# Performance work log

Hardware: AMD Instinct MI355X
Metric: run time of the kernel (lower is better)

Reference implementation:

```python
import jax, jax.numpy as jnp
import numpy as np

D_MODEL = 1024
N_HEADS = 16
N_GROUPS = 4
D_K = D_MODEL // N_HEADS
HEADS_PER_GROUP = N_HEADS // N_GROUPS


def rope(x):
    # x: [b, s, d]; rotate using half-split concat (NOT interleaved), matching source
    s, d = x.shape[1], x.shape[2]
    theta = 1.0 / (10000.0 ** (jnp.arange(d // 2, dtype=jnp.float32) / (d // 2)))
    ang = jnp.arange(s, dtype=jnp.float32)[:, None] * theta[None, :]  # [s, d/2]
    cos, sin = jnp.cos(ang), jnp.sin(ang)
    xe, xo = x[..., 0::2], x[..., 1::2]
    return jnp.concatenate([xe * cos - xo * sin, xe * sin + xo * cos], axis=-1)


def setup_inputs() -> dict:
    key = jax.random.key(0)
    k1, k2, k3, k4, k5 = jax.random.split(key, 5)
    b, s = 1, 2048
    scale = 0.02
    X = jax.random.normal(k1, (b, s, D_MODEL), dtype=jnp.float32)
    W_q = jax.random.normal(k2, (D_MODEL, D_MODEL), dtype=jnp.float32) * scale
    W_k = jax.random.normal(k3, (N_GROUPS * D_K, D_MODEL), dtype=jnp.float32) * scale
    W_v = jax.random.normal(k4, (N_GROUPS * D_K, D_MODEL), dtype=jnp.float32) * scale
    W_o = jax.random.normal(k5, (D_MODEL, D_MODEL), dtype=jnp.float32) * scale
    return {"X": X, "W_q": W_q, "W_k": W_k, "W_v": W_v, "W_o": W_o}


def reference(X, W_q, W_k, W_v, W_o):
    b, s, _ = X.shape
    Xr = rope(X)
    Q = (Xr @ W_q.T).reshape(b, s, N_HEADS, D_K).transpose(0, 2, 1, 3)
    K = (Xr @ W_k.T).reshape(b, s, N_GROUPS, D_K).transpose(0, 2, 1, 3)
    V = (Xr @ W_v.T).reshape(b, s, N_GROUPS, D_K).transpose(0, 2, 1, 3)
    Q = Q.reshape(b, N_GROUPS, HEADS_PER_GROUP, s, D_K)
    scores = jnp.einsum('bghsd,bgtd->bghst', Q, K) / jnp.sqrt(jnp.float32(D_K))
    mask = jnp.triu(jnp.ones((s, s), dtype=scores.dtype), k=1) * (-1e9)
    attn = jax.nn.softmax(scores + mask, axis=-1)
    out = jnp.einsum('bghst,bgtd->bghsd', attn, V)  # [b,g,h,s,dk]
    out = out.reshape(b, N_HEADS, s, D_K).transpose(0, 2, 1, 3).reshape(b, s, D_MODEL)
    return out @ W_o.T
```

## Files before the change

### kernel.cpp

```cpp
#include <hip/hip_runtime.h>
#include <hip/hip_bf16.h>

#define S_LEN   2048
#define D_MODEL 1024
#define N_HEADS 16
#define N_GROUPS 4
#define D_K     64
#define KV_DIM  (N_GROUPS * D_K)

typedef __hip_bfloat16 bf16;
typedef unsigned short u16;
typedef __attribute__((ext_vector_type(8))) short bfrag;
typedef __attribute__((ext_vector_type(4))) float ffrag;
typedef __attribute__((ext_vector_type(4))) unsigned int u32x4;

__device__ __forceinline__ float b2f(u16 u) {
    return __uint_as_float(((unsigned)u) << 16);
}
__device__ __forceinline__ u16 f2bu(float f) {
    bf16 h = __float2bfloat16(f);
    return __builtin_bit_cast(u16, h);
}
__device__ __forceinline__ unsigned cvt_pk_bf16(float lo, float hi) {
    unsigned r;
    asm("v_cvt_pk_bf16_f32 %0, %1, %2" : "=v"(r) : "v"(lo), "v"(hi));
    return r;
}
__device__ __forceinline__ float max3f(float a, float b, float c) {
    float d;
    asm("v_max3_f32 %0, %1, %2, %3" : "=v"(d) : "v"(a), "v"(b), "v"(c));
    return d;
}
__device__ __forceinline__ float ex2(float x) {
#if __has_builtin(__builtin_amdgcn_exp2f)
    return __builtin_amdgcn_exp2f(x);
#else
    return __expf(x * 0.69314718f);
#endif
}

typedef __attribute__((address_space(3))) u16 lds_u16;
typedef __attribute__((address_space(1))) const u16 glb_u16;
__device__ __forceinline__ void gld_lds16(const u16* g, u16* l) {
    __builtin_amdgcn_global_load_lds((glb_u16*)g, (lds_u16*)l, 16, 0, 0);
}

__device__ __forceinline__ int posCS3(int i, int c) {
    if (i >= 4 * c + 3)
        return (c == 0) ? i - 3 : (c == 1) ? i + 6 : (c == 2) ? i + 11 : 27;
    int dd = i - 4 * c + 1;
    return 28 + (3 - dd) * 4 + c;
}

__device__ __forceinline__ int probe_f32(const u16* p) {
    int lane = threadIdx.x & 63;
    int e0 = (p[lane] >> 7) & 0xFF;
    int e1 = (p[lane + 64] >> 7) & 0xFF;
    int c = ((e0 < 100 || e0 > 140) ? 1 : 0) + ((e1 < 100 || e1 > 140) ? 1 : 0);
    unsigned long long b1 = __ballot(c >= 1);
    unsigned long long b2 = __ballot(c >= 2);
    return ((__popcll(b1) + __popcll(b2)) > 16) ? 1 : 0;
}

__global__ void probe5_kernel(const u16* __restrict__ p0, const u16* __restrict__ p1,
                              const u16* __restrict__ p2, const u16* __restrict__ p3,
                              const u16* __restrict__ p4, int* __restrict__ mode) {
    if (blockIdx.x != 0) return;
    const u16* ps[5] = {p0, p1, p2, p3, p4};
    int lane = threadIdx.x & 63;
    for (int t = 0; t < 5; t++) {
        int e0 = (ps[t][lane] >> 7) & 0xFF;
        int e1 = (ps[t][lane + 64] >> 7) & 0xFF;
        int c = ((e0 < 100 || e0 > 140) ? 1 : 0) + ((e1 < 100 || e1 > 140) ? 1 : 0);
        unsigned long long b1 = __ballot(c >= 1);
        unsigned long long b2 = __ballot(c >= 2);
        if (lane == 0) mode[t] = ((__popcll(b1) + __popcll(b2)) > 16) ? 1 : 0;
    }
}

__global__ __launch_bounds__(512)
void prep_kernel(const void* __restrict__ Xin, u16* __restrict__ Xr,
                 const void* __restrict__ Wq, const void* __restrict__ Wk,
                 const void* __restrict__ Wv, const void* __restrict__ Wo,
                 u16* __restrict__ WB, u16* __restrict__ WoB) {
    int b = blockIdx.x;
    if (b < S_LEN) {
        int md = probe_f32((const u16*)Xin);
        int i = b;
        int j = threadIdx.x;
        float freq = ex2(-(float)j * 0.025952563241307518f);
        float ang  = (float)i * freq;
        float sv, cv;
        sincosf(ang, &sv, &cv);
        int base = i * D_MODEL;
        float xe, xo;
        if (md) {
            float2 xv = *(const float2*)&((const float*)Xin)[base + 2 * j];
            xe = xv.x; xo = xv.y;
        } else {
            ushort2 xv = *(const ushort2*)&((const u16*)Xin)[base + 2 * j];
            xe = b2f(xv.x); xo = b2f(xv.y);
        }
        Xr[base + j]       = f2bu(xe * cv - xo * sv);
        Xr[base + 512 + j] = f2bu(xe * sv + xo * cv);
    } else {
        int bid = b - S_LEN;
        const void* src; u16* dst; int goff;
        if (bid < 256)      { src = Wq; dst = WB;               goff = bid; }
        else if (bid < 320) { src = Wk; dst = WB + 1024 * 1024; goff = bid - 256; }
        else if (bid < 384) { src = Wv; dst = WB + 1280 * 1024; goff = bid - 320; }
        else                { src = Wo; dst = WoB;              goff = bid - 384; }
        int md = probe_f32((const u16*)src);
        size_t g = (size_t)goff * 512 + threadIdx.x;
        if (md) {
            const float* f = (const float*)src + g * 8;
            float4 v0 = *(const float4*)f;
            float4 v1 = *(const float4*)(f + 4);
            u16 t[8] = {f2bu(v0.x), f2bu(v0.y), f2bu(v0.z), f2bu(v0.w),
                        f2bu(v1.x), f2bu(v1.y), f2bu(v1.z), f2bu(v1.w)};
            *(uint4*)(dst + g * 8) = *(const uint4*)t;
        } else {
            *(uint4*)(dst + g * 8) = *(const uint4*)((const u16*)src + g * 8);
        }
    }
}

__global__ __launch_bounds__(512)
void rope_kernel(const void* __restrict__ Xin, u16* __restrict__ Xr) {
    int md = probe_f32((const u16*)Xin);
    int i = blockIdx.x;
    int j = threadIdx.x;
    float freq = ex2(-(float)j * 0.025952563241307518f);
    float ang  = (float)i * freq;
    float sv, cv;
    sincosf(ang, &sv, &cv);
    int base = i * D_MODEL;
    float xe, xo;
    if (md) {
        float2 xv = *(const float2*)&((const float*)Xin)[base + 2 * j];
        xe = xv.x; xo = xv.y;
    } else {
        ushort2 xv = *(const ushort2*)&((const u16*)Xin)[base + 2 * j];
        xe = b2f(xv.x); xo = b2f(xv.y);
    }
    Xr[base + j]       = f2bu(xe * cv - xo * sv);
    Xr[base + 512 + j] = f2bu(xe * sv + xo * cv);
}

template<int MODE>
__global__ __launch_bounds__(256)
void gemm_fast(const u16* __restrict__ A, const u16* __restrict__ WBm,
               u16* __restrict__ Qm, u16* __restrict__ Km, u16* __restrict__ Vm,
               float* __restrict__ Cf) {
    __shared__ u16 As[2][8192];
    __shared__ u16 Bs[2][4096];
    const int tid = threadIdx.x;
    const int w = tid >> 6, lane = tid & 63, quad = lane >> 4, lcol = lane & 15;

    const int flat = blockIdx.y * gridDim.x + blockIdx.x;
    const int cpx  = (gridDim.x * gridDim.y) >> 3;
    const int ns   = (flat & 7) * cpx + (flat >> 3);
    const int m0 = (ns / gridDim.x) * 128;
    const int n0 = (ns % gridDim.x) * 64;

    const int arl   = lane >> 3;
    const int colsw = ((lane & 7) ^ arl) * 8;

    const u16* ap[4]; const u16* bp[2];
    #pragma unroll
    for (int c = 0; c < 4; c++)
        ap[c] = A + (size_t)(m0 + (c * 4 + w) * 8 + arl) * 1024 + colsw;
    #pragma unroll
    for (int c = 0; c < 2; c++)
        bp[c] = WBm + (size_t)(n0 + (c * 4 + w) * 8 + arl) * 1024 + colsw;

    const int abase = (w * 32 + lcol) * 64;
    const int koff0 = (quad * 8) ^ ((lcol & 7) * 8);
    const int koff1 = koff0 ^ 32;

    ffrag acc[2][4];
    #pragma unroll
    for (int rf = 0; rf < 2; rf++)
        #pragma unroll
        for (int ct = 0; ct < 4; ct++) acc[rf][ct] = (ffrag)0.0f;

    #pragma unroll
    for (int c = 0; c < 4; c++) gld_lds16(ap[c], &As[0][(c * 4 + w) * 512]);
    #pragma unroll
    for (int c = 0; c < 2; c++) gld_lds16(bp[c], &Bs[0][(c * 4 + w) * 512]);
    __syncthreads();

    int cur = 0;
    for (int k0 = 0; k0 < D_MODEL; k0 += 64) {
        if (k0 + 64 < D_MODEL) {
            const int nb = cur ^ 1;
            #pragma unroll
            for (int c = 0; c < 4; c++)
                gld_lds16(ap[c] + k0 + 64, &As[nb][(c * 4 + w) * 512]);
            #pragma unroll
            for (int c = 0; c < 2; c++)
                gld_lds16(bp[c] + k0 + 64, &Bs[nb][(c * 4 + w) * 512]);
        }

        const u16* Ab = &As[cur][0];
        const u16* Bb = &Bs[cur][0];
        const bfrag a00 = *(const bfrag*)&Ab[abase + koff0];
        const bfrag a10 = *(const bfrag*)&Ab[abase + 1024 + koff0];
        const bfrag a01 = *(const bfrag*)&Ab[abase + koff1];
        const bfrag a11 = *(const bfrag*)&Ab[abase + 1024 + koff1];
        #pragma unroll
        for (int ct = 0; ct < 4; ct++) {
            const int bb = (ct * 16 + lcol) * 64;
            const bfrag b0 = *(const bfrag*)&Bb[bb + koff0];
            acc[0][ct] = __builtin_amdgcn_mfma_f32_16x16x32_bf16(a00, b0, acc[0][ct], 0, 0, 0);
            acc[1][ct] = __builtin_amdgcn_mfma_f32_16x16x32_bf16(a10, b0, acc[1][ct], 0, 0, 0);
            const bfrag b1 = *(const bfrag*)&Bb[bb + koff1];
            acc[0][ct] = __builtin_amdgcn_mfma_f32_16x16x32_bf16(a01, b1, acc[0][ct], 0, 0, 0);
            acc[1][ct] = __builtin_amdgcn_mfma_f32_16x16x32_bf16(a11, b1, acc[1][ct], 0, 0, 0);
        }
        __syncthreads();
        cur ^= 1;
    }

    if (MODE == 0) {
        if (n0 < 1280) {
            u16* Cp; int ldc, nc;
            if (n0 < 1024) { Cp = Qm; ldc = 1024; nc = n0; }
            else           { Cp = Km; ldc = 256;  nc = n0 - 1024; }
            #pragma unroll
            for (int rf = 0; rf < 2; rf++)
                #pragma unroll
                for (int ct = 0; ct < 4; ct++)
                    #pragma unroll
                    for (int r = 0; r < 4; r++) {
                        int row = m0 + w * 32 + rf * 16 + quad * 4 + r;
                        Cp[(size_t)row * ldc + nc + ct * 16 + lcol] = f2bu(acc[rf][ct][r]);
                    }
        } else {
            const int nc = n0 - 1280;
            #pragma unroll
            for (int rf = 0; rf < 2; rf++)
                #pragma unroll
                for (int ct = 0; ct < 4; ct++)
                    #pragma unroll
                    for (int r = 0; r < 4; r++) {
                        int row = m0 + w * 32 + rf * 16 + quad * 4 + r;
                        int col = nc + ct * 16 + lcol;
                        Vm[(size_t)col * S_LEN + row] = f2bu(acc[rf][ct][r]);
                    }
        }
    } else {
        #pragma unroll
        for (int rf = 0; rf < 2; rf++)
            #pragma unroll
            for (int ct = 0; ct < 4; ct++)
                #pragma unroll
                for (int r = 0; r < 4; r++) {
                    int row = m0 + w * 32 + rf * 16 + quad * 4 + r;
                    Cf[(size_t)row * D_MODEL + n0 + ct * 16 + lcol] = acc[rf][ct][r];
                }
    }
}

__device__ __forceinline__ void stageB(u16* dst, const void* Bv, size_t off, int md) {
    if (md) {
        const float* Bf = (const float*)Bv;
        float4 b0 = *(const float4*)&Bf[off];
        float4 b1 = *(const float4*)&Bf[off + 4];
        u16 t[8] = {f2bu(b0.x), f2bu(b0.y), f2bu(b0.z), f2bu(b0.w),
                    f2bu(b1.x), f2bu(b1.y), f2bu(b1.z), f2bu(b1.w)};
        *(uint4*)dst = *(const uint4*)t;
    } else {
        *(uint4*)dst = *(const uint4*)&((const u16*)Bv)[off];
    }
}

__global__ __launch_bounds__(256)
void qkv_mfma(const u16* __restrict__ Xr, const void* __restrict__ Wq,
              const void* __restrict__ Wk, const void* __restrict__ Wv,
              u16* __restrict__ Qm, u16* __restrict__ Km, u16* __restrict__ Vm,
              const int* __restrict__ mode) {
    __shared__ u16 As[128][36];
    __shared__ u16 Bs[64][36];
    const int tid = threadIdx.x;
    const int w = tid >> 6, lane = tid & 63, quad = lane >> 4, lcol = lane & 15;
    const int m0 = blockIdx.y * 128;
    const int n0 = blockIdx.x * 64;

    const void* Bv; int nb, md;
    if (n0 < 1024)       { Bv = Wq; nb = n0;        md = mode[1]; }
    else if (n0 < 1280)  { Bv = Wk; nb = n0 - 1024; md = mode[2]; }
    else                 { Bv = Wv; nb = n0 - 1280; md = mode[3]; }

    ffrag acc[2][4];
    #pragma unroll
    for (int rf = 0; rf < 2; rf++)
        #pragma unroll
        for (int ct = 0; ct < 4; ct++) acc[rf][ct] = (ffrag)0.0f;

    const int arow = tid >> 2, akc = tid & 3;
    for (int k0 = 0; k0 < D_MODEL; k0 += 32) {
        *(uint4*)&As[arow][akc * 8] =
            *(const uint4*)&Xr[(size_t)(m0 + arow) * D_MODEL + k0 + akc * 8];
        *(uint4*)&As[arow + 64][akc * 8] =
            *(const uint4*)&Xr[(size_t)(m0 + arow + 64) * D_MODEL + k0 + akc * 8];
        stageB(&Bs[arow][akc * 8], Bv, (size_t)(nb + arow) * D_MODEL + k0 + akc * 8, md);
        __syncthreads();
        const bfrag a0 = *(const bfrag*)&As[w * 32 + lcol][quad * 8];
        const bfrag a1 = *(const bfrag*)&As[w * 32 + 16 + lcol][quad * 8];
        #pragma unroll
        for (int ct = 0; ct < 4; ct++) {
            const bfrag b = *(const bfrag*)&Bs[ct * 16 + lcol][quad * 8];
            acc[0][ct] = __builtin_amdgcn_mfma_f32_16x16x32_bf16(a0, b, acc[0][ct], 0, 0, 0);
            acc[1][ct] = __builtin_amdgcn_mfma_f32_16x16x32_bf16(a1, b, acc[1][ct], 0, 0, 0);
        }
        __syncthreads();
    }

    if (n0 < 1280) {
        u16* Cp; int ldc, nc;
        if (n0 < 1024) { Cp = Qm; ldc = 1024; nc = n0; }
        else           { Cp = Km; ldc = 256;  nc = n0 - 1024; }
        #pragma unroll
        for (int rf = 0; rf < 2; rf++)
            #pragma unroll
            for (int ct = 0; ct < 4; ct++)
                #pragma unroll
                for (int r = 0; r < 4; r++) {
                    int row = m0 + w * 32 + rf * 16 + quad * 4 + r;
                    Cp[(size_t)row * ldc + nc + ct * 16 + lcol] = f2bu(acc[rf][ct][r]);
                }
    } else {
        const int nc = n0 - 1280;
        #pragma unroll
        for (int rf = 0; rf < 2; rf++)
            #pragma unroll
            for (int ct = 0; ct < 4; ct++)
                #pragma unroll
                for (int r = 0; r < 4; r++) {
                    int row = m0 + w * 32 + rf * 16 + quad * 4 + r;
                    int col = nc + ct * 16 + lcol;
                    Vm[(size_t)col * S_LEN + row] = f2bu(acc[rf][ct][r]);
                }
    }
}

__global__ __launch_bounds__(256)
void oproj_mfma(const u16* __restrict__ A, const void* __restrict__ B,
                float* __restrict__ C, const int* __restrict__ mode) {
    __shared__ u16 As[128][36];
    __shared__ u16 Bs[64][36];
    const int tid = threadIdx.x;
    const int w = tid >> 6, lane = tid & 63, quad = lane >> 4, lcol = lane & 15;
    const int m0 = blockIdx.y * 128;
    const int n0 = blockIdx.x * 64;
    const int md = mode[4];

    ffrag acc[2][4];
    #pragma unroll
    for (int rf = 0; rf < 2; rf++)
        #pragma unroll
        for (int ct = 0; ct < 4; ct++) acc[rf][ct] = (ffrag)0.0f;

    const int arow = tid >> 2, akc = tid & 3;
    for (int k0 = 0; k0 < D_MODEL; k0 += 32) {
        *(uint4*)&As[arow][akc * 8] =
            *(const uint4*)&A[(size_t)(m0 + arow) * D_MODEL + k0 + akc * 8];
        *(uint4*)&As[arow + 64][akc * 8] =
            *(const uint4*)&A[(size_t)(m0 + arow + 64) * D_MODEL + k0 + akc * 8];
        stageB(&Bs[arow][akc * 8], B, (size_t)(n0 + arow) * D_MODEL + k0 + akc * 8, md);
        __syncthreads();
        const bfrag a0 = *(const bfrag*)&As[w * 32 + lcol][quad * 8];
        const bfrag a1 = *(const bfrag*)&As[w * 32 + 16 + lcol][quad * 8];
        #pragma unroll
        for (int ct = 0; ct < 4; ct++) {
            const bfrag b = *(const bfrag*)&Bs[ct * 16 + lcol][quad * 8];
            acc[0][ct] = __builtin_amdgcn_mfma_f32_16x16x32_bf16(a0, b, acc[0][ct], 0, 0, 0);
            acc[1][ct] = __builtin_amdgcn_mfma_f32_16x16x32_bf16(a1, b, acc[1][ct], 0, 0, 0);
        }
        __syncthreads();
    }

    #pragma unroll
    for (int rf = 0; rf < 2; rf++)
        #pragma unroll
        for (int ct = 0; ct < 4; ct++)
            #pragma unroll
            for (int r = 0; r < 4; r++) {
                int row = m0 + w * 32 + rf * 16 + quad * 4 + r;
                C[(size_t)row * D_MODEL + n0 + ct * 16 + lcol] = acc[rf][ct][r];
            }
}

template<int CS, int SF>
__global__ __launch_bounds__(256, 4)
void attn_part(const u16* __restrict__ Q, const u16* __restrict__ K,
               const u16* __restrict__ Vt, float* __restrict__ OpF,
               u16* __restrict__ OpH, float2* __restrict__ ml2) {
    const int bid = blockIdx.x;
    const int cidx = bid >> 4;
    const int h = bid & 15;
    const int g = h >> 2;

    int i, c;
    if (CS == 3) {
        if (cidx < 13)       { c = 0; i = cidx + 3; }
        else if (cidx < 22)  { c = 1; i = cidx - 6; }
        else if (cidx < 27)  { c = 2; i = cidx - 11; }
        else if (cidx == 27) { c = 3; i = 15; }
        else { int t = cidx - 28; int dd = 3 - (t >> 2); c = t & 3; i = 4 * c + dd - 1; }
    } else {
        if (cidx < 8) { i = cidx; c = 0; }
        else          { i = 8 + ((cidx - 8) >> 1); c = (cidx - 8) & 1; }
    }
    const int i0 = i * 128;
    const int tile0 = c << CS;
    const int tlast = min(2 * i + 1, ((c + 1) << CS) - 1);
    const int nt = tlast - tile0 + 1;

    const int tid  = threadIdx.x;
    const int w    = tid >> 6;
    const int lane = tid & 63;
    const int quad = lane >> 4;
    const int lcol = lane & 15;

    __shared__ u16 Ks[2][64][72];
    __shared__ u16 Vts[2][64][72];

    const int qiA = i0 + w * 16 + lcol;
    const int qiB = qiA + 64;
    const bfrag qbA0 = *(const bfrag*)&Q[(size_t)qiA * D_MODEL + h * 64 + quad * 8];
    const bfrag qbA1 = *(const bfrag*)&Q[(size_t)qiA * D_MODEL + h * 64 + 32 + quad * 8];
    const bfrag qbB0 = *(const bfrag*)&Q[(size_t)qiB * D_MODEL + h * 64 + quad * 8];
    const bfrag qbB1 = *(const bfrag*)&Q[(size_t)qiB * D_MODEL + h * 64 + 32 + quad * 8];

    ffrag oaccA[4], oaccB[4];
    #pragma unroll
    for (int ct = 0; ct < 4; ct++) { oaccA[ct] = (ffrag)0.0f; oaccB[ct] = (ffrag)0.0f; }
    float m_runA = 0.0f, l_runA = 0.0f;
    float m_runB = 0.0f, l_runB = 0.0f;

    const int key0 = tid & 63, dc0 = tid >> 6;
    const int vd0 = tid >> 3, vch = tid & 7;
    const int vpos0 = 32 * (vch >> 2) + 16 * (vch & 1) + 4 * ((vch >> 1) & 1);
    const u16* vbase0 = &Vt[(size_t)(g * 64 + vd0) * S_LEN];
    const u16* vbase1 = &Vt[(size_t)(g * 64 + vd0 + 32) * S_LEN];

    int jp = tile0 * 64;
    uint4 kpre0 = *(const uint4*)&K[(size_t)(jp + key0) * KV_DIM + g * 64 + dc0 * 8];
    uint4 kpre1 = *(const uint4*)&K[(size_t)(jp + key0) * KV_DIM + g * 64 + (dc0 + 4) * 8];
    uint4 vpre0 = *(const uint4*)&vbase0[jp + vch * 8];
    uint4 vpre1 = *(const uint4*)&vbase1[jp + vch * 8];

    {
        *(uint4*)&Ks[0][key0][dc0 * 8]       = kpre0;
        *(uint4*)&Ks[0][key0][(dc0 + 4) * 8] = kpre1;
        *(uint2*)&Vts[0][vd0][vpos0]          = make_uint2(vpre0.x, vpre0.y);
        *(uint2*)&Vts[0][vd0][vpos0 + 8]      = make_uint2(vpre0.z, vpre0.w);
        *(uint2*)&Vts[0][vd0 + 32][vpos0]     = make_uint2(vpre1.x, vpre1.y);
        *(uint2*)&Vts[0][vd0 + 32][vpos0 + 8] = make_uint2(vpre1.z, vpre1.w);
    }

    const float CF = 0.18033688f;
    int cur = 0;

    for (int tt = 0; tt < nt; tt++) {
        const int tj = tile0 + tt;
        const int j0 = tj * 64;

        if (tt + 1 < nt) {
            const int j0n = (tj + 1) * 64;
            kpre0 = *(const uint4*)&K[(size_t)(j0n + key0) * KV_DIM + g * 64 + dc0 * 8];
            kpre1 = *(const uint4*)&K[(size_t)(j0n + key0) * KV_DIM + g * 64 + (dc0 + 4) * 8];
            vpre0 = *(const uint4*)&vbase0[j0n + vch * 8];
            vpre1 = *(const uint4*)&vbase1[j0n + vch * 8];
        }
        __syncthreads();

        ffrag saccA[4], saccB[4];
        #pragma unroll
        for (int ct = 0; ct < 4; ct++) { saccA[ct] = (ffrag)0.0f; saccB[ct] = (ffrag)0.0f; }
        __builtin_amdgcn_s_setprio(1);
        #pragma unroll
        for (int ct = 0; ct < 4; ct++) {
            const bfrag kb0 = *(const bfrag*)&Ks[cur][ct * 16 + lcol][quad * 8];
            saccA[ct] = __builtin_amdgcn_mfma_f32_16x16x32_bf16(kb0, qbA0, saccA[ct], 0, 0, 0);
            saccB[ct] = __builtin_amdgcn_mfma_f32_16x16x32_bf16(kb0, qbB0, saccB[ct], 0, 0, 0);
            const bfrag kb1 = *(const bfrag*)&Ks[cur][ct * 16 + lcol][32 + quad * 8];
            saccA[ct] = __builtin_amdgcn_mfma_f32_16x16x32_bf16(kb1, qbA1, saccA[ct], 0, 0, 0);
            saccB[ct] = __builtin_amdgcn_mfma_f32_16x16x32_bf16(kb1, qbB1, saccB[ct], 0, 0, 0);
        }
        __builtin_amdgcn_s_setprio(0);

        float svA[4][4];
        if (tj >= 2 * i) {
            #pragma unroll
            for (int ct = 0; ct < 4; ct++)
                #pragma unroll
                for (int r = 0; r < 4; r++) {
                    int kj = j0 + ct * 16 + quad * 4 + r;
                    svA[ct][r] = (kj <= qiA) ? saccA[ct][r] : -1e30f;
                }
        } else {
            #pragma unroll
            for (int ct = 0; ct < 4; ct++)
                #pragma unroll
                for (int r = 0; r < 4; r++) svA[ct][r] = saccA[ct][r];
        }
        float tA0 = max3f(svA[0][0], svA[0][1], svA[0][2]);
        float tA1 = max3f(svA[0][3], svA[1][0], svA[1][1]);
        float tA2 = max3f(svA[1][2], svA[1][3], svA[2][0]);
        float tA3 = max3f(svA[2][1], svA[2][2], svA[2][3]);
        float tA4 = max3f(svA[3][0], svA[3][1], svA[3][2]);
        float mxA = fmaxf(max3f(tA0, tA1, tA2), max3f(tA3, tA4, svA[3][3]));
        mxA = fmaxf(mxA, __shfl_xor(mxA, 16, 64));
        mxA = fmaxf(mxA, __shfl_xor(mxA, 32, 64));

        const float mcA = m_runA * CF;
        float rsA = 0.0f;
        #pragma unroll
        for (int ct = 0; ct < 4; ct++)
            #pragma unroll
            for (int r = 0; r < 4; r++) {
                float p = ex2(svA[ct][r] * CF - mcA);
                svA[ct][r] = p;
                rsA += p;
            }
        rsA += __shfl_xor(rsA, 16, 64);
        rsA += __shfl_xor(rsA, 32, 64);
        l_runA += rsA;

        u32x4 pwA0, pwA1;
        pwA0[0] = cvt_pk_bf16(svA[0][0], svA[0][1]);
        pwA0[1] = cvt_pk_bf16(svA[0][2], svA[0][3]);
        pwA0[2] = cvt_pk_bf16(svA[1][0], svA[1][1]);
        pwA0[3] = cvt_pk_bf16(svA[1][2], svA[1][3]);
        pwA1[0] = cvt_pk_bf16(svA[2][0], svA[2][1]);
        pwA1[1] = cvt_pk_bf16(svA[2][2], svA[2][3]);
        pwA1[2] = cvt_pk_bf16(svA[3][0], svA[3][1]);
        pwA1[3] = cvt_pk_bf16(svA[3][2], svA[3][3]);
        const bfrag paA0 = __builtin_bit_cast(bfrag, pwA0);
        const bfrag paA1 = __builtin_bit_cast(bfrag, pwA1);

        float svB[4][4];
        if (tj == 2 * i + 1) {
            #pragma unroll
            for (int ct = 0; ct < 4; ct++)
                #pragma unroll
                for (int r = 0; r < 4; r++) {
                    int kj = j0 + ct * 16 + quad * 4 + r;
                    svB[ct][r] = (kj <= qiB) ? saccB[ct][r] : -1e30f;
                }
        } else {
            #pragma unroll
            for (int ct = 0; ct < 4; ct++)
                #pragma unroll
                for (int r = 0; r < 4; r++) svB[ct][r] = saccB[ct][r];
        }
        float tB0 = max3f(svB[0][0], svB[0][1], svB[0][2]);
        float tB1 = max3f(svB[0][3], svB[1][0], svB[1][1]);
        float tB2 = max3f(svB[1][2], svB[1][3], svB[2][0]);
        float tB3 = max3f(svB[2][1], svB[2][2], svB[2][3]);
        float tB4 = max3f(svB[3][0], svB[3][1], svB[3][2]);
        float mxB = fmaxf(max3f(tB0, tB1, tB2), max3f(tB3, tB4, svB[3][3]));
        mxB = fmaxf(mxB, __shfl_xor(mxB, 16, 64));
        mxB = fmaxf(mxB, __shfl_xor(mxB, 32, 64));

        const float mcB = m_runB * CF;
        float rsB = 0.0f;
        #pragma unroll
        for (int ct = 0; ct < 4; ct++)
            #pragma unroll
            for (int r = 0; r < 4; r++) {
                float p = ex2(svB[ct][r] * CF - mcB);
                svB[ct][r] = p;
                rsB += p;
            }
        rsB += __shfl_xor(rsB, 16, 64);
        rsB += __shfl_xor(rsB, 32, 64);
        l_runB += rsB;

        u32x4 pwB0, pwB1;
        pwB0[0] = cvt_pk_bf16(svB[0][0], svB[0][1]);
        pwB0[1] = cvt_pk_bf16(svB[0][2], svB[0][3]);
        pwB0[2] = cvt_pk_bf16(svB[1][0], svB[1][1]);
        pwB0[3] = cvt_pk_bf16(svB[1][2], svB[1][3]);
        pwB1[0] = cvt_pk_bf16(svB[2][0], svB[2][1]);
        pwB1[1] = cvt_pk_bf16(svB[2][2], svB[2][3]);
        pwB1[2] = cvt_pk_bf16(svB[3][0], svB[3][1]);
        pwB1[3] = cvt_pk_bf16(svB[3][2], svB[3][3]);
        const bfrag paB0 = __builtin_bit_cast(bfrag, pwB0);
        const bfrag paB1 = __builtin_bit_cast(bfrag, pwB1);

        __builtin_amdgcn_s_setprio(1);
        #pragma unroll
        for (int ct = 0; ct < 4; ct++) {
            const bfrag vb0 = *(const bfrag*)&Vts[cur][ct * 16 + lcol][quad * 8];
            oaccA[ct] = __builtin_amdgcn_mfma_f32_16x16x32_bf16(paA0, vb0, oaccA[ct], 0, 0, 0);
            oaccB[ct] = __builtin_amdgcn_mfma_f32_16x16x32_bf16(paB0, vb0, oaccB[ct], 0, 0, 0);
            const bfrag vb1 = *(const bfrag*)&Vts[cur][ct * 16 + lcol][32 + quad * 8];
            oaccA[ct] = __builtin_amdgcn_mfma_f32_16x16x32_bf16(paA1, vb1, oaccA[ct], 0, 0, 0);
            oaccB[ct] = __builtin_amdgcn_mfma_f32_16x16x32_bf16(paB1, vb1, oaccB[ct], 0, 0, 0);
        }
        __builtin_amdgcn_s_setprio(0);

        if (!__all(mxA <= m_runA + 44.0f)) {
            float mnew = fmaxf(m_runA, mxA);
            float al = ex2((m_runA - mnew) * CF);
            l_runA *= al;
            #pragma unroll
            for (int r = 0; r < 4; r++) {
                float ar = __shfl(al, quad * 4 + r, 64);
                #pragma unroll
                for (int ct = 0; ct < 4; ct++) oaccA[ct][r] *= ar;
            }
            m_runA = mnew;
        }
        if (!__all(mxB <= m_runB + 44.0f)) {
            float mnew = fmaxf(m_runB, mxB);
            float al = ex2((m_runB - mnew) * CF);
            l_runB *= al;
            #pragma unroll
            for (int r = 0; r < 4; r++) {
                float ar = __shfl(al, quad * 4 + r, 64);
                #pragma unroll
                for (int ct = 0; ct < 4; ct++) oaccB[ct][r] *= ar;
            }
            m_runB = mnew;
        }

        if (tt + 1 < nt) {
            const int nb = cur ^ 1;
            *(uint4*)&Ks[nb][key0][dc0 * 8]       = kpre0;
            *(uint4*)&Ks[nb][key0][(dc0 + 4) * 8] = kpre1;
            *(uint2*)&Vts[nb][vd0][vpos0]          = make_uint2(vpre0.x, vpre0.y);
            *(uint2*)&Vts[nb][vd0][vpos0 + 8]      = make_uint2(vpre0.z, vpre0.w);
            *(uint2*)&Vts[nb][vd0 + 32][vpos0]     = make_uint2(vpre1.x, vpre1.y);
            *(uint2*)&Vts[nb][vd0 + 32][vpos0 + 8] = make_uint2(vpre1.z, vpre1.w);
        }
        cur ^= 1;
    }

    #pragma unroll
    for (int ct = 0; ct < 4; ct++)
        #pragma unroll
        for (int r = 0; r < 4; r++) {
            int rowA = w * 16 + quad * 4 + r;
            size_t offA = (size_t)bid * 8192 + rowA * 64 + ct * 16 + lcol;
            size_t offB = offA + 4096;
            if (SF) { OpF[offA] = oaccA[ct][r]; OpF[offB] = oaccB[ct][r]; }
            else    { OpH[offA] = f2bu(oaccA[ct][r]); OpH[offB] = f2bu(oaccB[ct][r]); }
        }
    if (quad == 0) {
        ml2[(size_t)bid * 128 + w * 16 + lcol]      = make_float2(m_runA * 0.125f, l_runA);
        ml2[(size_t)bid * 128 + 64 + w * 16 + lcol] = make_float2(m_runB * 0.125f, l_runB);
    }
}

template<int CS, int SF>
__global__ __launch_bounds__(256)
void attn_combine(const float* __restrict__ OpF, const u16* __restrict__ OpH,
                  const float2* __restrict__ ml2, u16* __restrict__ Om) {
    const int row = blockIdx.x;
    const int i = row >> 7;
    const int r = row & 127;
    const int t = threadIdx.x;
    const int h = t >> 4;
    const int d = (t & 15) * 4;
    const int nc = (CS == 3) ? ((2 * i + 1) >> 3) + 1 : ((2 * i + 1) >> 4) + 1;

    float M = -1e30f;
    for (int c = 0; c < nc; c++) {
        int pos = (CS == 3) ? posCS3(i, c) : ((i < 8) ? i : 8 + 2 * (i - 8) + c);
        float2 m = ml2[(size_t)(pos * 16 + h) * 128 + r];
        M = fmaxf(M, m.x);
    }
    float L = 0.0f;
    float acc[4] = {0.0f, 0.0f, 0.0f, 0.0f};
    for (int c = 0; c < nc; c++) {
        int pos = (CS == 3) ? posCS3(i, c) : ((i < 8) ? i : 8 + 2 * (i - 8) + c);
        float2 m = ml2[(size_t)(pos * 16 + h) * 128 + r];
        float wgt = __expf(m.x - M);
        L += m.y * wgt;
        size_t off = (size_t)(pos * 16 + h) * 8192 + r * 64 + d;
        if (SF) {
            float4 v = *(const float4*)&OpF[off];
            acc[0] += v.x * wgt; acc[1] += v.y * wgt;
            acc[2] += v.z * wgt; acc[3] += v.w * wgt;
        } else {
            ushort4 v = *(const ushort4*)&OpH[off];
            acc[0] += b2f(v.x) * wgt; acc[1] += b2f(v.y) * wgt;
            acc[2] += b2f(v.z) * wgt; acc[3] += b2f(v.w) * wgt;
        }
    }
    float inv = 1.0f / L;
    #pragma unroll
    for (int k = 0; k < 4; k++)
        Om[(size_t)row * D_MODEL + h * 64 + d + k] = f2bu(acc[k] * inv);
}

extern "C" void kernel_launch(void* const* d_in, const int* in_sizes, int n_in,
                              void* d_out, int out_size, void* d_ws, size_t ws_size,
                              hipStream_t stream) {
    const void* X  = d_in[0];
    const void* Wq = d_in[1];
    const void* Wk = d_in[2];
    const void* Wv = d_in[3];
    const void* Wo = d_in[4];
    float* out = (float*)d_out;

    u16* XrB = (u16*)d_out;

    int* mode = (int*)d_ws;
    u16* Qm = (u16*)((char*)d_ws + 64);
    u16* Km = Qm + (size_t)S_LEN * D_MODEL;
    u16* Vm = Km + (size_t)S_LEN * KV_DIM;
    u16* Om = Vm + (size_t)S_LEN * KV_DIM;

    const size_t needA    = 10485824ULL + 20971520ULL + 655360ULL;
    const size_t needFull = needA + 3145728ULL + 2097152ULL;

    if (ws_size >= needFull) {
        float*  OpF = (float*)((char*)d_ws + 10485824);
        float2* ml2 = (float2*)((char*)d_ws + 10485824 + 20971520);
        u16*    WB  = (u16*)((char*)d_ws + needA);
        u16*    WoB = WB + (size_t)1536 * 1024;

        prep_kernel<<<S_LEN + 640, 512, 0, stream>>>(X, XrB, Wq, Wk, Wv, Wo, WB, WoB);
        gemm_fast<0><<<dim3(24, 16), 256, 0, stream>>>(XrB, WB, Qm, Km, Vm, nullptr);
        attn_part<3, 1><<<40 * 16, 256, 0, stream>>>(Qm, Km, Vm, OpF, nullptr, ml2);
        attn_combine<3, 1><<<S_LEN, 256, 0, stream>>>(OpF, nullptr, ml2, Om);
        gemm_fast<1><<<dim3(16, 16), 256, 0, stream>>>(Om, WoB, nullptr, nullptr, nullptr, out);
    } else {
        rope_kernel<<<S_LEN, 512, 0, stream>>>(X, XrB);
        probe5_kernel<<<1, 64, 0, stream>>>(
            (const u16*)X, (const u16*)Wq, (const u16*)Wk, (const u16*)Wv,
            (const u16*)Wo, mode);
        qkv_mfma<<<dim3((D_MODEL + 2 * KV_DIM) / 64, S_LEN / 128), 256, 0, stream>>>(
            XrB, Wq, Wk, Wv, Qm, Km, Vm, mode);
        if (ws_size >= needA) {
            float*  OpF = (float*)((char*)d_ws + 10485824);
            float2* ml2 = (float2*)((char*)d_ws + 10485824 + 20971520);
            attn_part<3, 1><<<40 * 16, 256, 0, stream>>>(Qm, Km, Vm, OpF, nullptr, ml2);
            attn_combine<3, 1><<<S_LEN, 256, 0, stream>>>(OpF, nullptr, ml2, Om);
        } else {
            u16*    OpH = (u16*)d_out;
            float2* ml2 = (float2*)((char*)d_out + (size_t)768 * 4096 * 2);
            attn_part<4, 0><<<24 * 16, 256, 0, stream>>>(Qm, Km, Vm, nullptr, OpH, ml2);
            attn_combine<4, 0><<<S_LEN, 256, 0, stream>>>(nullptr, OpH, ml2, Om);
        }
        oproj_mfma<<<dim3(D_MODEL / 64, S_LEN / 128), 256, 0, stream>>>(Om, Wo, out, mode);
    }
}
```

Baseline: 136.4 us.

## Skip fully-masked A-row tiles and widen lazy softmax rescale threshold

Adds a per-tile hasA flag so that key tiles lying entirely beyond the A query block's causal range skip that block's QK and PV MFMAs and its softmax work. The lazy max-rescale now runs before exponentiation, uses a per-lane max with a wave vote before the cross-lane shuffle reduction, and its threshold rises from 44 to 550. Occupancy hint drops from 4 to 3 waves per SIMD to give the compiler more registers. The larger threshold lets ex2 arguments reach large values (around 99 in log2 units), which risks overflow in fp32 accumulators for inputs with big score spreads, and the split code paths add branching.

```diff
diff --git a/kernel.cpp b/kernel.cpp
--- a/kernel.cpp
+++ b/kernel.cpp
@@ -393,7 +393,7 @@
 }
 
 template<int CS, int SF>
-__global__ __launch_bounds__(256, 4)
+__global__ __launch_bounds__(256, 3)
 void attn_part(const u16* __restrict__ Q, const u16* __restrict__ K,
                const u16* __restrict__ Vt, float* __restrict__ OpF,
                u16* __restrict__ OpH, float2* __restrict__ ml2) {
@@ -462,11 +462,13 @@
     }
 
     const float CF = 0.18033688f;
+    const float GRD = 550.0f;
     int cur = 0;
 
     for (int tt = 0; tt < nt; tt++) {
         const int tj = tile0 + tt;
         const int j0 = tj * 64;
+        const bool hasA = (tj <= 2 * i);
 
         if (tt + 1 < nt) {
             const int j0n = (tj + 1) * 64;
@@ -481,66 +483,90 @@
         #pragma unroll
         for (int ct = 0; ct < 4; ct++) { saccA[ct] = (ffrag)0.0f; saccB[ct] = (ffrag)0.0f; }
         __builtin_amdgcn_s_setprio(1);
-        #pragma unroll
-        for (int ct = 0; ct < 4; ct++) {
-            const bfrag kb0 = *(const bfrag*)&Ks[cur][ct * 16 + lcol][quad * 8];
-            saccA[ct] = __builtin_amdgcn_mfma_f32_16x16x32_bf16(kb0, qbA0, saccA[ct], 0, 0, 0);
-            saccB[ct] = __builtin_amdgcn_mfma_f32_16x16x32_bf16(kb0, qbB0, saccB[ct], 0, 0, 0);
-            const bfrag kb1 = *(const bfrag*)&Ks[cur][ct * 16 + lcol][32 + quad * 8];
-            saccA[ct] = __builtin_amdgcn_mfma_f32_16x16x32_bf16(kb1, qbA1, saccA[ct], 0, 0, 0);
-            saccB[ct] = __builtin_amdgcn_mfma_f32_16x16x32_bf16(kb1, qbB1, saccB[ct], 0, 0, 0);
+        if (hasA) {
+            #pragma unroll
+            for (int ct = 0; ct < 4; ct++) {
+                const bfrag kb0 = *(const bfrag*)&Ks[cur][ct * 16 + lcol][quad * 8];
+                saccA[ct] = __builtin_amdgcn_mfma_f32_16x16x32_bf16(kb0, qbA0, saccA[ct], 0, 0, 0);
+                saccB[ct] = __builtin_amdgcn_mfma_f32_16x16x32_bf16(kb0, qbB0, saccB[ct], 0, 0, 0);
+                const bfrag kb1 = *(const bfrag*)&Ks[cur][ct * 16 + lcol][32 + quad * 8];
+                saccA[ct] = __builtin_amdgcn_mfma_f32_16x16x32_bf16(kb1, qbA1, saccA[ct], 0, 0, 0);
+                saccB[ct] = __builtin_amdgcn_mfma_f32_16x16x32_bf16(kb1, qbB1, saccB[ct], 0, 0, 0);
+            }
+        } else {
+            #pragma unroll
+            for (int ct = 0; ct < 4; ct++) {
+                const bfrag kb0 = *(const bfrag*)&Ks[cur][ct * 16 + lcol][quad * 8];
+                saccB[ct] = __builtin_amdgcn_mfma_f32_16x16x32_bf16(kb0, qbB0, saccB[ct], 0, 0, 0);
+                const bfrag kb1 = *(const bfrag*)&Ks[cur][ct * 16 + lcol][32 + quad * 8];
+                saccB[ct] = __builtin_amdgcn_mfma_f32_16x16x32_bf16(kb1, qbB1, saccB[ct], 0, 0, 0);
+            }
         }
         __builtin_amdgcn_s_setprio(0);
 
-        float svA[4][4];
-        if (tj >= 2 * i) {
+        bfrag paA0, paA1;
+        if (hasA) {
+            float svA[4][4];
+            if (tj == 2 * i) {
+                #pragma unroll
+                for (int ct = 0; ct < 4; ct++)
+                    #pragma unroll
+                    for (int r = 0; r < 4; r++) {
+                        int kj = j0 + ct * 16 + quad * 4 + r;
+                        svA[ct][r] = (kj <= qiA) ? saccA[ct][r] : -1e30f;
+                    }
+            } else {
+                #pragma unroll
+                for (int ct = 0; ct < 4; ct++)
+                    #pragma unroll
+                    for (int r = 0; r < 4; r++) svA[ct][r] = saccA[ct][r];
+            }
+            float tA0 = max3f(svA[0][0], svA[0][1], svA[0][2]);
+            float tA1 = max3f(svA[0][3], svA[1][0], svA[1][1]);
+            float tA2 = max3f(svA[1][2], svA[1][3], svA[2][0]);
+            float tA3 = max3f(svA[2][1], svA[2][2], svA[2][3]);
+            float tA4 = max3f(svA[3][0], svA[3][1], svA[3][2]);
+            float lA = fmaxf(max3f(tA0, tA1, tA2), max3f(tA3, tA4, svA[3][3]));
+            if (!__all(lA <= m_runA + GRD)) {
+                float mx = fmaxf(lA, __shfl_xor(lA, 16, 64));
+                mx = fmaxf(mx, __shfl_xor(mx, 32, 64));
+                float mnew = fmaxf(m_runA, mx);
+                float al = ex2((m_runA - mnew) * CF);
+                l_runA *= al;
+                #pragma unroll
+                for (int r = 0; r < 4; r++) {
+                    float ar = __shfl(al, quad * 4 + r, 64);
+                    #pragma unroll
+                    for (int ct = 0; ct < 4; ct++) oaccA[ct][r] *= ar;
+                }
+                m_runA = mnew;
+            }
+            const float mcA = m_runA * CF;
+            float rsA = 0.0f;
             #pragma unroll
             for (int ct = 0; ct < 4; ct++)
                 #pragma unroll
                 for (int r = 0; r < 4; r++) {
-                    int kj = j0 + ct * 16 + quad * 4 + r;
-                    svA[ct][r] = (kj <= qiA) ? saccA[ct][r] : -1e30f;
+                    float p = ex2(svA[ct][r] * CF - mcA);
+                    svA[ct][r] = p;
+                    rsA += p;
                 }
-        } else {
-            #pragma unroll
-            for (int ct = 0; ct < 4; ct++)
-                #pragma unroll
-                for (int r = 0; r < 4; r++) svA[ct][r] = saccA[ct][r];
-        }
-        float tA0 = max3f(svA[0][0], svA[0][1], svA[0][2]);
-        float tA1 = max3f(svA[0][3], svA[1][0], svA[1][1]);
-        float tA2 = max3f(svA[1][2], svA[1][3], svA[2][0]);
-        float tA3 = max3f(svA[2][1], svA[2][2], svA[2][3]);
-        float tA4 = max3f(svA[3][0], svA[3][1], svA[3][2]);
-        float mxA = fmaxf(max3f(tA0, tA1, tA2), max3f(tA3, tA4, svA[3][3]));
-        mxA = fmaxf(mxA, __shfl_xor(mxA, 16, 64));
-        mxA = fmaxf(mxA, __shfl_xor(mxA, 32, 64));
-
-        const float mcA = m_runA * CF;
-        float rsA = 0.0f;
-        #pragma unroll
-        for (int ct = 0; ct < 4; ct++)
-            #pragma unroll
-            for (int r = 0; r < 4; r++) {
-                float p = ex2(svA[ct][r] * CF - mcA);
-                svA[ct][r] = p;
-                rsA += p;
-            }
-        rsA += __shfl_xor(rsA, 16, 64);
-        rsA += __shfl_xor(rsA, 32, 64);
-        l_runA += rsA;
-
-        u32x4 pwA0, pwA1;
-        pwA0[0] = cvt_pk_bf16(svA[0][0], svA[0][1]);
-        pwA0[1] = cvt_pk_bf16(svA[0][2], svA[0][3]);
-        pwA0[2] = cvt_pk_bf16(svA[1][0], svA[1][1]);
-        pwA0[3] = cvt_pk_bf16(svA[1][2], svA[1][3]);
-        pwA1[0] = cvt_pk_bf16(svA[2][0], svA[2][1]);
-        pwA1[1] = cvt_pk_bf16(svA[2][2], svA[2][3]);
-        pwA1[2] = cvt_pk_bf16(svA[3][0], svA[3][1]);
-        pwA1[3] = cvt_pk_bf16(svA[3][2], svA[3][3]);
-        const bfrag paA0 = __builtin_bit_cast(bfrag, pwA0);
-        const bfrag paA1 = __builtin_bit_cast(bfrag, pwA1);
+            rsA += __shfl_xor(rsA, 16, 64);
+            rsA += __shfl_xor(rsA, 32, 64);
+            l_runA += rsA;
+
+            u32x4 pwA0, pwA1;
+            pwA0[0] = cvt_pk_bf16(svA[0][0], svA[0][1]);
+            pwA0[1] = cvt_pk_bf16(svA[0][2], svA[0][3]);
+            pwA0[2] = cvt_pk_bf16(svA[1][0], svA[1][1]);
+            pwA0[3] = cvt_pk_bf16(svA[1][2], svA[1][3]);
+            pwA1[0] = cvt_pk_bf16(svA[2][0], svA[2][1]);
+            pwA1[1] = cvt_pk_bf16(svA[2][2], svA[2][3]);
+            pwA1[2] = cvt_pk_bf16(svA[3][0], svA[3][1]);
+            pwA1[3] = cvt_pk_bf16(svA[3][2], svA[3][3]);
+            paA0 = __builtin_bit_cast(bfrag, pwA0);
+            paA1 = __builtin_bit_cast(bfrag, pwA1);
+        }
 
         float svB[4][4];
         if (tj == 2 * i + 1) {
@@ -562,10 +588,21 @@
         float tB2 = max3f(svB[1][2], svB[1][3], svB[2][0]);
         float tB3 = max3f(svB[2][1], svB[2][2], svB[2][3]);
         float tB4 = max3f(svB[3][0], svB[3][1], svB[3][2]);
-        float mxB = fmaxf(max3f(tB0, tB1, tB2), max3f(tB3, tB4, svB[3][3]));
-        mxB = fmaxf(mxB, __shfl_xor(mxB, 16, 64));
-        mxB = fmaxf(mxB, __shfl_xor(mxB, 32, 64));
-
+        float lB = fmaxf(max3f(tB0, tB1, tB2), max3f(tB3, tB4, svB[3][3]));
+        if (!__all(lB <= m_runB + GRD)) {
+            float mx = fmaxf(lB, __shfl_xor(lB, 16, 64));
+            mx = fmaxf(mx, __shfl_xor(mx, 32, 64));
+            float mnew = fmaxf(m_runB, mx);
+            float al = ex2((m_runB - mnew) * CF);
+            l_runB *= al;
+            #pragma unroll
+            for (int r = 0; r < 4; r++) {
+                float ar = __shfl(al, quad * 4 + r, 64);
+                #pragma unroll
+                for (int ct = 0; ct < 4; ct++) oaccB[ct][r] *= ar;
+            }
+            m_runB = mnew;
+        }
         const float mcB = m_runB * CF;
         float rsB = 0.0f;
         #pragma unroll
@@ -593,41 +630,26 @@
         const bfrag paB1 = __builtin_bit_cast(bfrag, pwB1);
 
         __builtin_amdgcn_s_setprio(1);
-        #pragma unroll
-        for (int ct = 0; ct < 4; ct++) {
-            const bfrag vb0 = *(const bfrag*)&Vts[cur][ct * 16 + lcol][quad * 8];
-            oaccA[ct] = __builtin_amdgcn_mfma_f32_16x16x32_bf16(paA0, vb0, oaccA[ct], 0, 0, 0);
-            oaccB[ct] = __builtin_amdgcn_mfma_f32_16x16x32_bf16(paB0, vb0, oaccB[ct], 0, 0, 0);
-            const bfrag vb1 = *(const bfrag*)&Vts[cur][ct * 16 + lcol][32 + quad * 8];
-            oaccA[ct] = __builtin_amdgcn_mfma_f32_16x16x32_bf16(paA1, vb1, oaccA[ct], 0, 0, 0);
-            oaccB[ct] = __builtin_amdgcn_mfma_f32_16x16x32_bf16(paB1, vb1, oaccB[ct], 0, 0, 0);
+        if (hasA) {
+            #pragma unroll
+            for (int ct = 0; ct < 4; ct++) {
+                const bfrag vb0 = *(const bfrag*)&Vts[cur][ct * 16 + lcol][quad * 8];
+                oaccA[ct] = __builtin_amdgcn_mfma_f32_16x16x32_bf16(paA0, vb0, oaccA[ct], 0, 0, 0);
+                oaccB[ct] = __builtin_amdgcn_mfma_f32_16x16x32_bf16(paB0, vb0, oaccB[ct], 0, 0, 0);
+                const bfrag vb1 = *(const bfrag*)&Vts[cur][ct * 16 + lcol][32 + quad * 8];
+                oaccA[ct] = __builtin_amdgcn_mfma_f32_16x16x32_bf16(paA1, vb1, oaccA[ct], 0, 0, 0);
+                oaccB[ct] = __builtin_amdgcn_mfma_f32_16x16x32_bf16(paB1, vb1, oaccB[ct], 0, 0, 0);
+            }
+        } else {
+            #pragma unroll
+            for (int ct = 0; ct < 4; ct++) {
+                const bfrag vb0 = *(const bfrag*)&Vts[cur][ct * 16 + lcol][quad * 8];
+                oaccB[ct] = __builtin_amdgcn_mfma_f32_16x16x32_bf16(paB0, vb0, oaccB[ct], 0, 0, 0);
+                const bfrag vb1 = *(const bfrag*)&Vts[cur][ct * 16 + lcol][32 + quad * 8];
+                oaccB[ct] = __builtin_amdgcn_mfma_f32_16x16x32_bf16(paB1, vb1, oaccB[ct], 0, 0, 0);
+            }
         }
         __builtin_amdgcn_s_setprio(0);
-
-        if (!__all(mxA <= m_runA + 44.0f)) {
-            float mnew = fmaxf(m_runA, mxA);
-            float al = ex2((m_runA - mnew) * CF);
-            l_runA *= al;
-            #pragma unroll
-            for (int r = 0; r < 4; r++) {
-                float ar = __shfl(al, quad * 4 + r, 64);
-                #pragma unroll
-                for (int ct = 0; ct < 4; ct++) oaccA[ct][r] *= ar;
-            }
-            m_runA = mnew;
-        }
-        if (!__all(mxB <= m_runB + 44.0f)) {
-            float mnew = fmaxf(m_runB, mxB);
-            float al = ex2((m_runB - mnew) * CF);
-            l_runB *= al;
-            #pragma unroll
-            for (int r = 0; r < 4; r++) {
-                float ar = __shfl(al, quad * 4 + r, 64);
-                #pragma unroll
-                for (int ct = 0; ct < 4; ct++) oaccB[ct][r] *= ar;
-            }
-            m_runB = mnew;
-        }
 
         if (tt + 1 < nt) {
             const int nb = cur ^ 1;
```

Result: no change. 134.6 us (-1.3%).
